# Performance work log

Measured on AMD Instinct MI355X. Metric: run time of the kernel, lower is better.

The kernel has to match this reference:

```python
import jax, jax.numpy as jnp
import numpy as np

B, S, D, H = 2, 2048, 768, 12
DK = D // H

def setup_inputs() -> dict:
    key = jax.random.key(0)
    ks = jax.random.split(key, 5)
    scale = 1.0 / np.sqrt(D)
    return {
        "X": jax.random.normal(ks[0], (B, S, D), dtype=jnp.float32),
        "Wq": jax.random.normal(ks[1], (D, D), dtype=jnp.float32) * scale,
        "Wk": jax.random.normal(ks[2], (D, D), dtype=jnp.float32) * scale,
        "Wv": jax.random.normal(ks[3], (D, D), dtype=jnp.float32) * scale,
        "Wo": jax.random.normal(ks[4], (D, D), dtype=jnp.float32) * scale,
    }

def reference(X, Wq, Wk, Wv, Wo):
    # torch Linear: y = x @ W.T  (no bias in this repo's Linear)
    Q = X @ Wq.T  # (B,S,D)
    K = X @ Wk.T
    V = X @ Wv.T
    def split_heads(t):
        return t.reshape(B, S, H, DK).transpose(0, 2, 1, 3)  # (B,H,S,DK)
    Qh, Kh, Vh = split_heads(Q), split_heads(K), split_heads(V)
    scores = jnp.einsum('bhqd,bhkd->bhqk', Qh, Kh) / jnp.sqrt(jnp.float32(DK))
    causal = jnp.tril(jnp.ones((S, S), dtype=bool))  # keep lower triangle
    scores = jnp.where(causal, scores, -jnp.inf)
    attn = jax.nn.softmax(scores, axis=-1)
    out_h = jnp.einsum('bhqk,bhkd->bhqd', attn, Vh)  # (B,H,S,DK)
    out = out_h.transpose(0, 2, 1, 3).reshape(B, S, D)
    return out @ Wo.T
```

## Files before the change

### kernel.cpp

```cpp
#include <hip/hip_runtime.h>
#include <stdint.h>

#define BB   2
#define SS   2048
#define DD   768
#define HH   12
#define MM   (BB*SS)
#define XSZ  (MM*DD)
#define WSZ  (DD*DD)

typedef __bf16 v8bf __attribute__((ext_vector_type(8)));
typedef float  v4f  __attribute__((ext_vector_type(4)));

__device__ inline v4f mfma16(v8bf a, v8bf b, v4f c) {
    return __builtin_amdgcn_mfma_f32_16x16x32_bf16(a, b, c, 0, 0, 0);
}

__device__ inline unsigned short f2bf(float f) {
    union { float f; uint32_t u; } v; v.f = f;
    return (unsigned short)((v.u + 0x7FFFu + ((v.u >> 16) & 1u)) >> 16);
}

__device__ inline uint4 cvt8(const float* __restrict__ p) {
    uint4 out;
    unsigned short* s = (unsigned short*)&out;
#pragma unroll
    for (int j = 0; j < 8; ++j) s[j] = f2bf(p[j]);
    return out;
}

__device__ __forceinline__ void gld_lds16(const unsigned short* g, unsigned short* l) {
    __builtin_amdgcn_global_load_lds(
        (const __attribute__((address_space(1))) void*)g,
        (__attribute__((address_space(3))) void*)l, 16, 0, 0);
}

__global__ __launch_bounds__(256) void gemm_qkv64f(
    const float* __restrict__ X,
    const float* __restrict__ Wq,
    const float* __restrict__ Wk,
    const float* __restrict__ Wv,
    unsigned short* __restrict__ Qo,
    unsigned short* __restrict__ Ko,
    unsigned short* __restrict__ Vo)
{
    __shared__ __align__(16) unsigned short As[64 * 64];
    __shared__ __align__(16) unsigned short Bs[3][64 * 64];

    const int flat = (int)(blockIdx.y * gridDim.x + blockIdx.x);
    const int sw   = (flat & 7) * 96 + (flat >> 3);
    const int m0   = (sw / 12) * 64;
    const int n0   = (sw % 12) * 64;

    const int tid  = threadIdx.x;
    const int wave = tid >> 6, lane = tid & 63;
    const int quad = lane >> 4, l16 = lane & 15;
    const int waveM = (wave >> 1) * 32, waveN = (wave & 1) * 32;

    const int rA  = tid >> 2;
    const int cA  = (tid & 3) * 16;
    const int rxA = (rA & 7) << 4;
    const int swz = (l16 & 7) << 4;

    v4f acc[3][2][2] = {};

    const float* ap = X  + (size_t)(m0 + rA) * DD + cA;
    const float* w0 = Wq + (size_t)(n0 + rA) * DD + cA;
    const float* w1 = Wk + (size_t)(n0 + rA) * DD + cA;
    const float* w2 = Wv + (size_t)(n0 + rA) * DD + cA;

    for (int kt = 0; kt < DD; kt += 64) {
        __syncthreads();
        *(uint4*)((char*)As + rA * 128 + ((cA * 2)      ^ rxA)) = cvt8(ap + kt);
        *(uint4*)((char*)As + rA * 128 + ((cA * 2 + 16) ^ rxA)) = cvt8(ap + kt + 8);
        *(uint4*)((char*)&Bs[0][0] + rA * 128 + ((cA * 2)      ^ rxA)) = cvt8(w0 + kt);
        *(uint4*)((char*)&Bs[0][0] + rA * 128 + ((cA * 2 + 16) ^ rxA)) = cvt8(w0 + kt + 8);
        *(uint4*)((char*)&Bs[1][0] + rA * 128 + ((cA * 2)      ^ rxA)) = cvt8(w1 + kt);
        *(uint4*)((char*)&Bs[1][0] + rA * 128 + ((cA * 2 + 16) ^ rxA)) = cvt8(w1 + kt + 8);
        *(uint4*)((char*)&Bs[2][0] + rA * 128 + ((cA * 2)      ^ rxA)) = cvt8(w2 + kt);
        *(uint4*)((char*)&Bs[2][0] + rA * 128 + ((cA * 2 + 16) ^ rxA)) = cvt8(w2 + kt + 8);
        __syncthreads();

        v8bf af[2][2];
#pragma unroll
        for (int mi = 0; mi < 2; ++mi) {
            const char* arow = (const char*)As + (size_t)(waveM + mi * 16 + l16) * 128;
#pragma unroll
            for (int kf = 0; kf < 2; ++kf)
                af[mi][kf] = *(const v8bf*)(arow + ((kf * 64 + quad * 16) ^ swz));
        }
#pragma unroll
        for (int z = 0; z < 3; ++z) {
            v8bf bfr[2][2];
#pragma unroll
            for (int ni = 0; ni < 2; ++ni) {
                const char* brow = (const char*)&Bs[z][0] + (size_t)(waveN + ni * 16 + l16) * 128;
#pragma unroll
                for (int kf = 0; kf < 2; ++kf)
                    bfr[ni][kf] = *(const v8bf*)(brow + ((kf * 64 + quad * 16) ^ swz));
            }
#pragma unroll
            for (int mi = 0; mi < 2; ++mi)
#pragma unroll
                for (int ni = 0; ni < 2; ++ni) {
                    acc[z][mi][ni] = mfma16(af[mi][0], bfr[ni][0], acc[z][mi][ni]);
                    acc[z][mi][ni] = mfma16(af[mi][1], bfr[ni][1], acc[z][mi][ni]);
                }
        }
    }

#pragma unroll
    for (int mi = 0; mi < 2; ++mi)
#pragma unroll
        for (int ni = 0; ni < 2; ++ni)
#pragma unroll
            for (int r = 0; r < 4; ++r) {
                const int row = m0 + waveM + mi * 16 + quad * 4 + r;
                const int col = n0 + waveN + ni * 16 + l16;
                Qo[(size_t)row * DD + col] = f2bf(acc[0][mi][ni][r]);
                Ko[(size_t)row * DD + col] = f2bf(acc[1][mi][ni][r]);
                const int b = row >> 11, s = row & 2047;
                const int h = col >> 6,  dk = col & 63;
                Vo[(((size_t)(b * HH + h)) * 64 + dk) * SS + s] = f2bf(acc[2][mi][ni][r]);
            }
}

__global__ __launch_bounds__(256) void gemm_of(
    const unsigned short* __restrict__ A,
    const float* __restrict__ W,
    float* __restrict__ C)
{
    __shared__ __align__(16) unsigned short As[2][64 * 64];
    __shared__ __align__(16) unsigned short Bs[2][64 * 64];

    const int flat = (int)(blockIdx.y * gridDim.x + blockIdx.x);
    const int sw   = (flat & 7) * 96 + (flat >> 3);
    const int m0   = (sw / 12) * 64;
    const int n0   = (sw % 12) * 64;

    const int tid  = threadIdx.x;
    const int wave = tid >> 6, lane = tid & 63;
    const int quad = lane >> 4, l16 = lane & 15;
    const int waveM = (wave >> 1) * 32, waveN = (wave & 1) * 32;

    const int rB  = wave * 8 + (lane >> 3);
    const int cB  = ((lane & 7) ^ (lane >> 3)) * 8;
    const int rW  = tid >> 2;
    const int cW  = (tid & 3) * 16;
    const int rxW = (rW & 7) << 4;
    const int swz = (l16 & 7) << 4;

    const unsigned short* a0 = A + (size_t)(m0 + rB) * DD + cB;
    const float*          b0 = W + (size_t)(n0 + rW) * DD + cW;

    v4f acc[2][2] = {};

    gld_lds16(a0,           &As[0][wave * 512]);
    gld_lds16(a0 + 32 * DD, &As[0][2048 + wave * 512]);
    *(uint4*)((char*)&Bs[0][0] + rW * 128 + ((cW * 2)      ^ rxW)) = cvt8(b0);
    *(uint4*)((char*)&Bs[0][0] + rW * 128 + ((cW * 2 + 16) ^ rxW)) = cvt8(b0 + 8);
    __syncthreads();

    int cur = 0;
    for (int kt = 0; kt < DD; kt += 64) {
        if (kt + 64 < DD) {
            gld_lds16(a0 + kt + 64,           &As[cur ^ 1][wave * 512]);
            gld_lds16(a0 + kt + 64 + 32 * DD, &As[cur ^ 1][2048 + wave * 512]);
            *(uint4*)((char*)&Bs[cur ^ 1][0] + rW * 128 + ((cW * 2)      ^ rxW)) = cvt8(b0 + kt + 64);
            *(uint4*)((char*)&Bs[cur ^ 1][0] + rW * 128 + ((cW * 2 + 16) ^ rxW)) = cvt8(b0 + kt + 64 + 8);
        }
#pragma unroll
        for (int kf = 0; kf < 2; ++kf) {
            v8bf af[2], bfr[2];
#pragma unroll
            for (int i = 0; i < 2; ++i) {
                af[i]  = *(const v8bf*)((const char*)&As[cur][0] +
                          (size_t)(waveM + i * 16 + l16) * 128 + ((kf * 64 + quad * 16) ^ swz));
                bfr[i] = *(const v8bf*)((const char*)&Bs[cur][0] +
                          (size_t)(waveN + i * 16 + l16) * 128 + ((kf * 64 + quad * 16) ^ swz));
            }
#pragma unroll
            for (int mi = 0; mi < 2; ++mi)
#pragma unroll
                for (int ni = 0; ni < 2; ++ni)
                    acc[mi][ni] = mfma16(af[mi], bfr[ni], acc[mi][ni]);
        }
        __syncthreads();
        cur ^= 1;
    }

#pragma unroll
    for (int mi = 0; mi < 2; ++mi)
#pragma unroll
        for (int ni = 0; ni < 2; ++ni)
#pragma unroll
            for (int r = 0; r < 4; ++r) {
                const int row = m0 + waveM + mi * 16 + quad * 4 + r;
                const int col = n0 + waveN + ni * 16 + l16;
                C[(size_t)row * DD + col] = acc[mi][ni][r];
            }
}

__global__ __launch_bounds__(256, 3) void attn_ls(
    const unsigned short* Q,
    const unsigned short* __restrict__ Kg,
    const unsigned short* __restrict__ Vt,
    unsigned short* O)
{
    const int h = blockIdx.x, b = blockIdx.y;
    const int qs = (SS / 64 - 1 - (int)blockIdx.z) * 64;
    const int tid  = threadIdx.x;
    const int wave = tid >> 6, lane = tid & 63;
    const int quad = lane >> 4, l16 = lane & 15;
    const int qw = qs + wave * 16;
    const float scale = 0.125f;

    __shared__ __align__(16) unsigned short Ks[2][4096];
    __shared__ __align__(16) unsigned short Vs[2][4096];
    __shared__ __align__(16) unsigned short Ps[4][16 * 72];

    v8bf qf0, qf1;
    {
        const unsigned short* qp = &Q[((size_t)(b * SS + qw + l16)) * DD + h * 64];
        qf0 = *(const v8bf*)(qp + quad * 8);
        qf1 = *(const v8bf*)(qp + 32 + quad * 8);
    }

    const int NT = qs / 64 + 1;
    const char* kgb = (const char*)&Kg[(size_t)(b * SS) * DD + h * 64];
    const char* vgb = (const char*)&Vt[((size_t)(b * HH + h) * 64) * SS];

    const int rA = wave * 8 + (lane >> 3);
    const int oA = ((lane & 7) * 16) ^ ((rA & 7) << 4);
    const int swz = (l16 & 7) << 4;

    v4f oacc[4] = {};
    float l_run[4] = {0.f, 0.f, 0.f, 0.f};
    unsigned short* pw = &Ps[wave][0];

    gld_lds16((const unsigned short*)(kgb + (size_t)rA        * (DD * 2) + oA), &Ks[0][wave * 512]);
    gld_lds16((const unsigned short*)(kgb + (size_t)(rA + 32) * (DD * 2) + oA), &Ks[0][2048 + wave * 512]);
    gld_lds16((const unsigned short*)(vgb + (size_t)rA        * (SS * 2) + oA), &Vs[0][wave * 512]);
    gld_lds16((const unsigned short*)(vgb + (size_t)(rA + 32) * (SS * 2) + oA), &Vs[0][2048 + wave * 512]);
    __syncthreads();

    for (int kt = 0; kt < NT; ++kt) {
        const int cur = kt & 1;
        const int kb  = kt * 64;

        if (kt + 1 < NT) {
            const size_t kb2 = (size_t)(kb + 64);
            gld_lds16((const unsigned short*)(kgb + (kb2 + rA)      * (DD * 2) + oA), &Ks[cur ^ 1][wave * 512]);
            gld_lds16((const unsigned short*)(kgb + (kb2 + rA + 32) * (DD * 2) + oA), &Ks[cur ^ 1][2048 + wave * 512]);
            gld_lds16((const unsigned short*)(vgb + (size_t)rA        * (SS * 2) + kb2 * 2 + oA), &Vs[cur ^ 1][wave * 512]);
            gld_lds16((const unsigned short*)(vgb + (size_t)(rA + 32) * (SS * 2) + kb2 * 2 + oA), &Vs[cur ^ 1][2048 + wave * 512]);
        }

        const char* ksb = (const char*)&Ks[cur][0];
        const char* vsb = (const char*)&Vs[cur][0];

        v8bf kf0[4], kf1[4];
#pragma unroll
        for (int nk = 0; nk < 4; ++nk) {
            const char* krow = ksb + (size_t)(nk * 16 + l16) * 128;
            kf0[nk] = *(const v8bf*)(krow + ((quad * 16) ^ swz));
            kf1[nk] = *(const v8bf*)(krow + ((64 + quad * 16) ^ swz));
        }

        v4f sacc[4] = {};
#pragma unroll
        for (int nk = 0; nk < 4; ++nk) {
            sacc[nk] = mfma16(qf0, kf0[nk], sacc[nk]);
            sacc[nk] = mfma16(qf1, kf1[nk], sacc[nk]);
        }

        const bool diag = (kt == NT - 1);
        float pv[4][4];
#pragma unroll
        for (int nk = 0; nk < 4; ++nk)
#pragma unroll
            for (int r = 0; r < 4; ++r) {
                float p = __expf(sacc[nk][r] * scale);
                if (diag) {
                    int key  = kb + nk * 16 + l16;
                    int qrow = qw + quad * 4 + r;
                    if (key > qrow) p = 0.0f;
                }
                pv[nk][r] = p;
                l_run[r] += p;
            }

        v8bf vf[2][4];
#pragma unroll
        for (int kc = 0; kc < 2; ++kc)
#pragma unroll
            for (int dt = 0; dt < 4; ++dt) {
                const char* vr = vsb + (size_t)(dt * 16 + l16) * 128;
                vf[kc][dt] = *(const v8bf*)(vr + ((kc * 64 + quad * 16) ^ swz));
            }

#pragma unroll
        for (int nk = 0; nk < 4; ++nk)
#pragma unroll
            for (int r = 0; r < 4; ++r)
                pw[(quad * 4 + r) * 72 + nk * 16 + l16] = f2bf(pv[nk][r]);
        __asm__ volatile("" ::: "memory");

        v8bf pa0 = *(const v8bf*)(&pw[l16 * 72 + quad * 8]);
        v8bf pa1 = *(const v8bf*)(&pw[l16 * 72 + 32 + quad * 8]);
#pragma unroll
        for (int dt = 0; dt < 4; ++dt) oacc[dt] = mfma16(pa0, vf[0][dt], oacc[dt]);
#pragma unroll
        for (int dt = 0; dt < 4; ++dt) oacc[dt] = mfma16(pa1, vf[1][dt], oacc[dt]);

        __syncthreads();
    }

    for (int off = 1; off < 16; off <<= 1)
#pragma unroll
        for (int r = 0; r < 4; ++r)
            l_run[r] += __shfl_xor(l_run[r], off, 64);

    float inv[4];
#pragma unroll
    for (int r = 0; r < 4; ++r) inv[r] = 1.0f / l_run[r];

    unsigned short* ob = &O[((size_t)(b * SS + qw + quad * 4)) * DD + h * 64 + l16];
#pragma unroll
    for (int r = 0; r < 4; ++r)
#pragma unroll
        for (int dt = 0; dt < 4; ++dt)
            ob[(size_t)r * DD + dt * 16] = f2bf(oacc[dt][r] * inv[r]);
}

extern "C" void kernel_launch(void* const* d_in, const int* in_sizes, int n_in,
                              void* d_out, int out_size, void* d_ws, size_t ws_size,
                              hipStream_t stream)
{
    const float* X  = (const float*)d_in[0];
    const float* Wq = (const float*)d_in[1];
    const float* Wk = (const float*)d_in[2];
    const float* Wv = (const float*)d_in[3];
    const float* Wo = (const float*)d_in[4];
    float* Out = (float*)d_out;

    unsigned short* Qb  = (unsigned short*)d_ws;
    unsigned short* Kb  = Qb + XSZ;
    unsigned short* Vtb = (unsigned short*)d_out;

    dim3 blk(256);

    dim3 g1(DD / 64, MM / 64);
    gemm_qkv64f<<<g1, blk, 0, stream>>>(X, Wq, Wk, Wv, Qb, Kb, Vtb);

    dim3 g2(HH, BB, SS / 64);
    attn_ls<<<g2, blk, 0, stream>>>(Qb, Kb, Vtb, Qb);

    dim3 g3(DD / 64, MM / 64);
    gemm_of<<<g3, blk, 0, stream>>>(Qb, Wo, Out);
}
```

Before: 166.5 us.

## Pre-convert QKV weights to bf16 and load B tiles directly into LDS

Adds a small kernel that converts Wq, Wk and Wv to bf16 once per call, writing them into spare space in the output buffer. The QKV GEMM then fetches weight tiles with global_load_lds (direct global-to-LDS) using an XOR-swizzled column mapping, in place of per-thread fp32 loads followed by bf16 conversion and LDS stores. This removes the weight conversion that every M-block used to repeat and halves the bytes read for weights. In exchange it adds one extra kernel launch and a global write and read of the converted weights.

New measurement: 153.8 us. 7.6% less time.

```diff
diff --git a/kernel.cpp b/kernel.cpp
--- a/kernel.cpp
+++ b/kernel.cpp
@@ -35,11 +35,25 @@
         (__attribute__((address_space(3))) void*)l, 16, 0, 0);
 }
 
-__global__ __launch_bounds__(256) void gemm_qkv64f(
+__global__ __launch_bounds__(256) void cvt_w3(
+    const float* __restrict__ Wq, const float* __restrict__ Wk,
+    const float* __restrict__ Wv, unsigned short* __restrict__ dst)
+{
+    long i4 = ((long)blockIdx.x * 256 + threadIdx.x) * 4;
+    int t = (int)(i4 / WSZ);
+    long off = i4 - (long)t * WSZ;
+    const float* s = (t == 0) ? Wq : (t == 1) ? Wk : Wv;
+    float4 v = *(const float4*)(s + off);
+    ushort4 o;
+    o.x = f2bf(v.x); o.y = f2bf(v.y); o.z = f2bf(v.z); o.w = f2bf(v.w);
+    *(ushort4*)(dst + (size_t)t * WSZ + off) = o;
+}
+
+__global__ __launch_bounds__(256) void gemm_qkv64(
     const float* __restrict__ X,
-    const float* __restrict__ Wq,
-    const float* __restrict__ Wk,
-    const float* __restrict__ Wv,
+    const unsigned short* __restrict__ Wq,
+    const unsigned short* __restrict__ Wk,
+    const unsigned short* __restrict__ Wv,
     unsigned short* __restrict__ Qo,
     unsigned short* __restrict__ Ko,
     unsigned short* __restrict__ Vo)
@@ -60,25 +74,28 @@
     const int rA  = tid >> 2;
     const int cA  = (tid & 3) * 16;
     const int rxA = (rA & 7) << 4;
+
+    const int rB  = wave * 8 + (lane >> 3);
+    const int cB  = ((lane & 7) ^ (lane >> 3)) * 8;
     const int swz = (l16 & 7) << 4;
 
     v4f acc[3][2][2] = {};
 
-    const float* ap = X  + (size_t)(m0 + rA) * DD + cA;
-    const float* w0 = Wq + (size_t)(n0 + rA) * DD + cA;
-    const float* w1 = Wk + (size_t)(n0 + rA) * DD + cA;
-    const float* w2 = Wv + (size_t)(n0 + rA) * DD + cA;
+    const float* ap0 = X + (size_t)(m0 + rA) * DD + cA;
+    const unsigned short* w0 = Wq + (size_t)(n0 + rB) * DD + cB;
+    const unsigned short* w1 = Wk + (size_t)(n0 + rB) * DD + cB;
+    const unsigned short* w2 = Wv + (size_t)(n0 + rB) * DD + cB;
 
     for (int kt = 0; kt < DD; kt += 64) {
         __syncthreads();
-        *(uint4*)((char*)As + rA * 128 + ((cA * 2)      ^ rxA)) = cvt8(ap + kt);
-        *(uint4*)((char*)As + rA * 128 + ((cA * 2 + 16) ^ rxA)) = cvt8(ap + kt + 8);
-        *(uint4*)((char*)&Bs[0][0] + rA * 128 + ((cA * 2)      ^ rxA)) = cvt8(w0 + kt);
-        *(uint4*)((char*)&Bs[0][0] + rA * 128 + ((cA * 2 + 16) ^ rxA)) = cvt8(w0 + kt + 8);
-        *(uint4*)((char*)&Bs[1][0] + rA * 128 + ((cA * 2)      ^ rxA)) = cvt8(w1 + kt);
-        *(uint4*)((char*)&Bs[1][0] + rA * 128 + ((cA * 2 + 16) ^ rxA)) = cvt8(w1 + kt + 8);
-        *(uint4*)((char*)&Bs[2][0] + rA * 128 + ((cA * 2)      ^ rxA)) = cvt8(w2 + kt);
-        *(uint4*)((char*)&Bs[2][0] + rA * 128 + ((cA * 2 + 16) ^ rxA)) = cvt8(w2 + kt + 8);
+        *(uint4*)((char*)As + rA * 128 + ((cA * 2)      ^ rxA)) = cvt8(ap0 + kt);
+        *(uint4*)((char*)As + rA * 128 + ((cA * 2 + 16) ^ rxA)) = cvt8(ap0 + kt + 8);
+        gld_lds16(w0 + kt,           &Bs[0][wave * 512]);
+        gld_lds16(w0 + kt + 32 * DD, &Bs[0][2048 + wave * 512]);
+        gld_lds16(w1 + kt,           &Bs[1][wave * 512]);
+        gld_lds16(w1 + kt + 32 * DD, &Bs[1][2048 + wave * 512]);
+        gld_lds16(w2 + kt,           &Bs[2][wave * 512]);
+        gld_lds16(w2 + kt + 32 * DD, &Bs[2][2048 + wave * 512]);
         __syncthreads();
 
         v8bf af[2][2];
@@ -347,11 +364,15 @@
     unsigned short* Qb  = (unsigned short*)d_ws;
     unsigned short* Kb  = Qb + XSZ;
     unsigned short* Vtb = (unsigned short*)d_out;
+    unsigned short* Wqb = Vtb + XSZ;
 
     dim3 blk(256);
 
+    cvt_w3<<<1728, blk, 0, stream>>>(Wq, Wk, Wv, Wqb);
+
     dim3 g1(DD / 64, MM / 64);
-    gemm_qkv64f<<<g1, blk, 0, stream>>>(X, Wq, Wk, Wv, Qb, Kb, Vtb);
+    gemm_qkv64<<<g1, blk, 0, stream>>>(X, Wqb, Wqb + WSZ, Wqb + 2 * WSZ,
+                                       Qb, Kb, Vtb);
 
     dim3 g2(HH, BB, SS / 64);
     attn_ls<<<g2, blk, 0, stream>>>(Qb, Kb, Vtb, Qb);
```
